# Optimization experiments

Hardware: AMD Instinct MI355X
Metric: run time of the kernel (lower is better)

Reference implementation:

```python
import jax, jax.numpy as jnp
import numpy as np

N_Q = 4
DEPTH = 6
DIM = 16  # 2**N_Q

# ---- fixed `design` dict (forward arg in the torch module; fixed here so the
# gate sequence is static, exercising every gate branch) ----
_K1 = ['x', 'y', 'z']
_K2 = ['H', 'Px', 'Py', 'Pz', 'CNot', 'CZ', 'Tof', 'CSwap']
DESIGN = {}
for _l in range(DEPTH):
    for _n in range(N_Q):
        DESIGN[str(_l) + str(_n) + '0'] = ((_l + _n) % 2 == 0)
        DESIGN[str(_l) + str(_n) + '1'] = _K1[(_l + _n) % 3]
        DESIGN[str(_l) + str(_n) + '2'] = _K2[(_l * N_Q + _n) % 8]

# ---- elementary gate matrices (numpy, build-time) ----
_H = np.array([[1, 1], [1, -1]], np.complex64) / np.sqrt(2.0)
_X = np.array([[0, 1], [1, 0]], np.complex64)
_Y = np.array([[0, -1j], [1j, 0]], np.complex64)
_Z = np.array([[1, 0], [0, -1]], np.complex64)
_CNOT = np.eye(4, dtype=np.complex64)[[0, 1, 3, 2]]
_CZ = np.diag(np.array([1, 1, 1, -1], np.complex64))
_TOF = np.eye(8, dtype=np.complex64)[[0, 1, 2, 3, 4, 5, 7, 6]]
_CSWAP = np.eye(8, dtype=np.complex64)[[0, 1, 2, 3, 4, 6, 5, 7]]


def _embed(gate, wires):
    # Embed a 2^k x 2^k gate acting on `wires` (wire 0 = most-significant bit,
    # PennyLane convention) into a full 16x16 unitary.
    k = len(wires)
    U = np.zeros((DIM, DIM), np.complex64)
    for i in range(DIM):
        bits = [(i >> (N_Q - 1 - q)) & 1 for q in range(N_Q)]
        sub_in = 0
        for w in wires:
            sub_in = (sub_in << 1) | bits[w]
        for sub_out in range(2 ** k):
            amp = gate[sub_out, sub_in]
            if amp != 0:
                ob = list(bits)
                for j, w in enumerate(wires):
                    ob[w] = (sub_out >> (k - 1 - j)) & 1
                o = 0
                for q in range(N_Q):
                    o = (o << 1) | ob[q]
                U[o, i] += amp
    return jnp.asarray(U)


# ---- static op list: ('fix', U16) | ('rot', kind, wire, angle_source) ----
_G1 = {'H': _H, 'Px': _X, 'Py': _Y, 'Pz': _Z}
OPS = [('fix', _embed(_H, [q])) for q in range(N_Q)]  # initial Hadamards
for _l in range(DEPTH):
    for _n in range(N_Q):
        if DESIGN[str(_l) + str(_n) + '0']:
            OPS.append(('rot', 'y', _n, ('x', _n)))  # RY(input feature)
        OPS.append(('rot', DESIGN[str(_l) + str(_n) + '1'], _n, ('w', _l, _n)))
        g = DESIGN[str(_l) + str(_n) + '2']
        if g in _G1:
            OPS.append(('fix', _embed(_G1[g], [_n])))
        elif g == 'CNot':
            OPS.append(('fix', _embed(_CNOT, [_n, (_n + 1) % N_Q])))
        elif g == 'CZ':
            OPS.append(('fix', _embed(_CZ, [_n, (_n + 1) % N_Q])))
        elif g == 'Tof':
            OPS.append(('fix', _embed(_TOF, [_n, (_n + 1) % N_Q, (_n + 2) % N_Q])))
        elif g == 'CSwap':
            OPS.append(('fix', _embed(_CSWAP, [_n, (_n + 1) % N_Q, (_n + 2) % N_Q])))


def _rot_mat(kind, th):
    # th: (B,) real angles -> (B,2,2) complex64 rotation matrices
    half = 0.5 * th
    c = jnp.cos(half).astype(jnp.complex64)
    s = jnp.sin(half).astype(jnp.complex64)
    if kind == 'x':
        m = [[c, (-1j) * s], [(-1j) * s, c]]
    elif kind == 'y':
        m = [[c, -s], [s, c]]
    else:  # 'z'
        e = jnp.exp((-1j) * half.astype(jnp.complex64))
        z = jnp.zeros_like(e)
        m = [[e, z], [z, jnp.conj(e)]]
    return jnp.stack([jnp.stack(m[0], -1), jnp.stack(m[1], -1)], -2)


def _apply_1q(state, M, q):
    # state: (B,16) complex, M: (B,2,2) complex, single-qubit gate on wire q
    B = state.shape[0]
    s = state.reshape(B, 2 ** q, 2, 2 ** (N_Q - 1 - q))
    s = jnp.einsum('bij,bajc->baic', M, s)
    return s.reshape(B, DIM)


def _run(state, x, w, adjoint):
    # adjoint: reversed gate order, negated rotation angles; all fixed gates
    # here (H, Paulis, CNOT, CZ, Toffoli, CSWAP) are Hermitian => self-adjoint.
    sign = -1.0 if adjoint else 1.0
    B = state.shape[0]
    for op in (reversed(OPS) if adjoint else OPS):
        if op[0] == 'fix':
            state = jnp.einsum('ij,bj->bi', op[1], state)
        else:
            _, kind, wire, src = op
            th = x[:, src[1]] if src[0] == 'x' else jnp.broadcast_to(w[src[1], src[2]], (B,))
            state = _apply_1q(state, _rot_mat(kind, sign * th), wire)
    return state


def _forward(x1, x2, q_params):
    w = q_params.reshape(DEPTH, N_Q)
    B = x1.shape[0]
    state = jnp.zeros((B, DIM), jnp.complex64).at[:, 0].set(1.0)
    state = _run(state, x1, w, False)   # quantum_net(x1, w)
    state = _run(state, x2, w, True)    # adjoint(quantum_net)(x2, w)
    a = state[:, 0]                     # probs[0] = |<0...0|psi>|^2
    return a.real ** 2 + a.imag ** 2


def setup_inputs():
    key = jax.random.key(0)
    k1, k2, k3 = jax.random.split(key, 3)
    B = 262144
    return {
        'x1': jax.random.normal(k1, (B, N_Q), jnp.float32),
        'x2': jax.random.normal(k2, (B, N_Q), jnp.float32),
        'q_params': jax.random.normal(k3, (DEPTH * N_Q,), jnp.float32),
    }


def reference(x1, x2, q_params):
    return _forward(x1, x2, q_params)
```

## Files before the change

### kernel.cpp

```cpp
#include <hip/hip_runtime.h>
#include <math.h>


#define DEVI static __device__ __forceinline__


template<int Q> DEVI void gH(float* vr, float* vi) {
  constexpr int m = 1 << (3 - Q);
  const float K = 0.70710678118654752440f;
#pragma unroll
  for (int i = 0; i < 16; ++i) if (!(i & m)) {
    const int j = i | m;
    float ar = vr[i], ai = vi[i], br = vr[j], bi = vi[j];
    vr[i] = (ar + br) * K; vi[i] = (ai + bi) * K;
    vr[j] = (ar - br) * K; vi[j] = (ai - bi) * K;
  }
}

template<int Q> DEVI void gX(float* vr, float* vi) {
  constexpr int m = 1 << (3 - Q);
#pragma unroll
  for (int i = 0; i < 16; ++i) if (!(i & m)) {
    const int j = i | m; float t;
    t = vr[i]; vr[i] = vr[j]; vr[j] = t;
    t = vi[i]; vi[i] = vi[j]; vi[j] = t;
  }
}

template<int Q> DEVI void gY(float* vr, float* vi) {
  constexpr int m = 1 << (3 - Q);
#pragma unroll
  for (int i = 0; i < 16; ++i) if (!(i & m)) {
    const int j = i | m;
    float ar = vr[i], ai = vi[i], br = vr[j], bi = vi[j];
    vr[i] = bi;  vi[i] = -br;
    vr[j] = -ai; vi[j] = ar;
  }
}

template<int Q> DEVI void gZ(float* vr, float* vi) {
  constexpr int m = 1 << (3 - Q);
#pragma unroll
  for (int i = 0; i < 16; ++i) if (i & m) { vr[i] = -vr[i]; vi[i] = -vi[i]; }
}

template<int Q> DEVI void gRY(float* vr, float* vi, float c, float s) {
  constexpr int m = 1 << (3 - Q);
#pragma unroll
  for (int i = 0; i < 16; ++i) if (!(i & m)) {
    const int j = i | m;
    float ar = vr[i], ai = vi[i], br = vr[j], bi = vi[j];
    vr[i] = c * ar - s * br; vi[i] = c * ai - s * bi;
    vr[j] = s * ar + c * br; vi[j] = s * ai + c * bi;
  }
}

template<int Q> DEVI void gRX(float* vr, float* vi, float c, float s) {
  constexpr int m = 1 << (3 - Q);
#pragma unroll
  for (int i = 0; i < 16; ++i) if (!(i & m)) {
    const int j = i | m;
    float ar = vr[i], ai = vi[i], br = vr[j], bi = vi[j];
    vr[i] = c * ar + s * bi; vi[i] = c * ai - s * br;
    vr[j] = c * br + s * ai; vi[j] = c * bi - s * ar;
  }
}

template<int Q> DEVI void gRZ(float* vr, float* vi, float c, float s) {
  constexpr int m = 1 << (3 - Q);
#pragma unroll
  for (int i = 0; i < 16; ++i) {
    float ar = vr[i], ai = vi[i];
    if (i & m) { vr[i] = c * ar - s * ai; vi[i] = c * ai + s * ar; }
    else       { vr[i] = c * ar + s * ai; vi[i] = c * ai - s * ar; }
  }
}

template<int C, int T> DEVI void gCNOT(float* vr, float* vi) {
  constexpr int mc = 1 << (3 - C), mt = 1 << (3 - T);
#pragma unroll
  for (int i = 0; i < 16; ++i) if ((i & mc) && !(i & mt)) {
    const int j = i | mt; float t;
    t = vr[i]; vr[i] = vr[j]; vr[j] = t;
    t = vi[i]; vi[i] = vi[j]; vi[j] = t;
  }
}

template<int A, int B2> DEVI void gCZ(float* vr, float* vi) {
  constexpr int ma = 1 << (3 - A), mb = 1 << (3 - B2);
#pragma unroll
  for (int i = 0; i < 16; ++i) if ((i & ma) && (i & mb)) { vr[i] = -vr[i]; vi[i] = -vi[i]; }
}

template<int C1, int C2, int T> DEVI void gTOF(float* vr, float* vi) {
  constexpr int m1 = 1 << (3 - C1), m2 = 1 << (3 - C2), mt = 1 << (3 - T);
#pragma unroll
  for (int i = 0; i < 16; ++i) if ((i & m1) && (i & m2) && !(i & mt)) {
    const int j = i | mt; float t;
    t = vr[i]; vr[i] = vr[j]; vr[j] = t;
    t = vi[i]; vi[i] = vi[j]; vi[j] = t;
  }
}

template<int C, int A, int B2> DEVI void gCSWAP(float* vr, float* vi) {
  constexpr int mc = 1 << (3 - C), ma = 1 << (3 - A), mb = 1 << (3 - B2);
#pragma unroll
  for (int i = 0; i < 16; ++i) if ((i & mc) && (i & ma) && !(i & mb)) {
    const int j = (i ^ ma) | mb; float t;
    t = vr[i]; vr[i] = vr[j]; vr[j] = t;
    t = vi[i]; vi[i] = vi[j]; vi[j] = t;
  }
}

__global__ void qprep(const float* __restrict__ q, float* __restrict__ wcs) {
  int k = threadIdx.x;
  if (k < 24) {
    float s, c;
    sincosf(0.5f * q[k], &s, &c);
    wcs[k] = c; wcs[24 + k] = s;
  }
}

template<bool WSPRE>
__global__ __launch_bounds__(256)
void qsim(const float* __restrict__ x1, const float* __restrict__ x2,
          const float* __restrict__ q, const float* __restrict__ wcs,
          float* __restrict__ out, int B)
{
  const int b = blockIdx.x * blockDim.x + threadIdx.x;
  if (b >= B) return;

  float cw[24], sw[24];
  if constexpr (WSPRE) {
#pragma unroll
    for (int k = 0; k < 24; ++k) { cw[k] = wcs[k]; sw[k] = wcs[24 + k]; }
  } else {
#pragma unroll
    for (int k = 0; k < 24; ++k) sincosf(0.5f * q[k], &sw[k], &cw[k]);
  }

  const float4 xa = reinterpret_cast<const float4*>(x1)[b];
  const float4 xb = reinterpret_cast<const float4*>(x2)[b];
  float ca[4], sa[4], cb[4], sb[4];
  sincosf(0.5f * xa.x, &sa[0], &ca[0]);
  sincosf(0.5f * xa.y, &sa[1], &ca[1]);
  sincosf(0.5f * xa.z, &sa[2], &ca[2]);
  sincosf(0.5f * xa.w, &sa[3], &ca[3]);
  sincosf(0.5f * xb.x, &sb[0], &cb[0]);
  sincosf(0.5f * xb.y, &sb[1], &cb[1]);
  sincosf(0.5f * xb.z, &sb[2], &cb[2]);
  sincosf(0.5f * xb.w, &sb[3], &cb[3]);

  float vr[16], vi[16];
#pragma unroll
  for (int i = 0; i < 16; ++i) { vr[i] = 0.f; vi[i] = 0.f; }
  vr[0] = 1.f;

  gH<0>(vr, vi); gH<1>(vr, vi); gH<2>(vr, vi); gH<3>(vr, vi);
  gRY<0>(vr, vi, ca[0], sa[0]); gRX<0>(vr, vi, cw[0],  sw[0]);  gH<0>(vr, vi);
  gRY<1>(vr, vi, cw[1], sw[1]); gX<1>(vr, vi);
  gRY<2>(vr, vi, ca[2], sa[2]); gRZ<2>(vr, vi, cw[2],  sw[2]);  gY<2>(vr, vi);
  gRX<3>(vr, vi, cw[3], sw[3]); gZ<3>(vr, vi);
  gRY<0>(vr, vi, cw[4], sw[4]); gCNOT<0,1>(vr, vi);
  gRY<1>(vr, vi, ca[1], sa[1]); gRZ<1>(vr, vi, cw[5],  sw[5]);  gCZ<1,2>(vr, vi);
  gRX<2>(vr, vi, cw[6], sw[6]); gTOF<2,3,0>(vr, vi);
  gRY<3>(vr, vi, ca[3], sa[3]); gRY<3>(vr, vi, cw[7],  sw[7]);  gCSWAP<3,0,1>(vr, vi);
  gRY<0>(vr, vi, ca[0], sa[0]); gRZ<0>(vr, vi, cw[8],  sw[8]);  gH<0>(vr, vi);
  gRX<1>(vr, vi, cw[9], sw[9]); gX<1>(vr, vi);
  gRY<2>(vr, vi, ca[2], sa[2]); gRY<2>(vr, vi, cw[10], sw[10]); gY<2>(vr, vi);
  gRZ<3>(vr, vi, cw[11], sw[11]); gZ<3>(vr, vi);
  gRX<0>(vr, vi, cw[12], sw[12]); gCNOT<0,1>(vr, vi);
  gRY<1>(vr, vi, ca[1], sa[1]); gRY<1>(vr, vi, cw[13], sw[13]); gCZ<1,2>(vr, vi);
  gRZ<2>(vr, vi, cw[14], sw[14]); gTOF<2,3,0>(vr, vi);
  gRY<3>(vr, vi, ca[3], sa[3]); gRX<3>(vr, vi, cw[15], sw[15]); gCSWAP<3,0,1>(vr, vi);
  gRY<0>(vr, vi, ca[0], sa[0]); gRY<0>(vr, vi, cw[16], sw[16]); gH<0>(vr, vi);
  gRZ<1>(vr, vi, cw[17], sw[17]); gX<1>(vr, vi);
  gRY<2>(vr, vi, ca[2], sa[2]); gRX<2>(vr, vi, cw[18], sw[18]); gY<2>(vr, vi);
  gRY<3>(vr, vi, cw[19], sw[19]); gZ<3>(vr, vi);
  gRZ<0>(vr, vi, cw[20], sw[20]); gCNOT<0,1>(vr, vi);
  gRY<1>(vr, vi, ca[1], sa[1]); gRX<1>(vr, vi, cw[21], sw[21]); gCZ<1,2>(vr, vi);
  gRY<2>(vr, vi, cw[22], sw[22]); gTOF<2,3,0>(vr, vi);
  gRY<3>(vr, vi, ca[3], sa[3]); gRZ<3>(vr, vi, cw[23], sw[23]); gCSWAP<3,0,1>(vr, vi);

  gCSWAP<3,0,1>(vr, vi); gRZ<3>(vr, vi, cw[23], -sw[23]); gRY<3>(vr, vi, cb[3], -sb[3]);
  gTOF<2,3,0>(vr, vi);   gRY<2>(vr, vi, cw[22], -sw[22]);
  gCZ<1,2>(vr, vi);      gRX<1>(vr, vi, cw[21], -sw[21]); gRY<1>(vr, vi, cb[1], -sb[1]);
  gCNOT<0,1>(vr, vi);    gRZ<0>(vr, vi, cw[20], -sw[20]);
  gZ<3>(vr, vi); gRY<3>(vr, vi, cw[19], -sw[19]);
  gY<2>(vr, vi); gRX<2>(vr, vi, cw[18], -sw[18]); gRY<2>(vr, vi, cb[2], -sb[2]);
  gX<1>(vr, vi); gRZ<1>(vr, vi, cw[17], -sw[17]);
  gH<0>(vr, vi); gRY<0>(vr, vi, cw[16], -sw[16]); gRY<0>(vr, vi, cb[0], -sb[0]);
  gCSWAP<3,0,1>(vr, vi); gRX<3>(vr, vi, cw[15], -sw[15]); gRY<3>(vr, vi, cb[3], -sb[3]);
  gTOF<2,3,0>(vr, vi);   gRZ<2>(vr, vi, cw[14], -sw[14]);
  gCZ<1,2>(vr, vi);      gRY<1>(vr, vi, cw[13], -sw[13]); gRY<1>(vr, vi, cb[1], -sb[1]);
  gCNOT<0,1>(vr, vi);    gRX<0>(vr, vi, cw[12], -sw[12]);
  gZ<3>(vr, vi); gRZ<3>(vr, vi, cw[11], -sw[11]);
  gY<2>(vr, vi); gRY<2>(vr, vi, cw[10], -sw[10]); gRY<2>(vr, vi, cb[2], -sb[2]);
  gX<1>(vr, vi); gRX<1>(vr, vi, cw[9],  -sw[9]);
  gH<0>(vr, vi); gRZ<0>(vr, vi, cw[8],  -sw[8]);  gRY<0>(vr, vi, cb[0], -sb[0]);
  gCSWAP<3,0,1>(vr, vi); gRY<3>(vr, vi, cw[7], -sw[7]); gRY<3>(vr, vi, cb[3], -sb[3]);
  gTOF<2,3,0>(vr, vi);   gRX<2>(vr, vi, cw[6], -sw[6]);
  gCZ<1,2>(vr, vi);      gRZ<1>(vr, vi, cw[5], -sw[5]); gRY<1>(vr, vi, cb[1], -sb[1]);
  gCNOT<0,1>(vr, vi);    gRY<0>(vr, vi, cw[4], -sw[4]);
  gZ<3>(vr, vi); gRX<3>(vr, vi, cw[3], -sw[3]);
  gY<2>(vr, vi); gRZ<2>(vr, vi, cw[2], -sw[2]); gRY<2>(vr, vi, cb[2], -sb[2]);
  gX<1>(vr, vi); gRY<1>(vr, vi, cw[1], -sw[1]);
  gH<0>(vr, vi); gRX<0>(vr, vi, cw[0], -sw[0]); gRY<0>(vr, vi, cb[0], -sb[0]);
  gH<3>(vr, vi); gH<2>(vr, vi); gH<1>(vr, vi); gH<0>(vr, vi);

  out[b] = vr[0] * vr[0] + vi[0] * vi[0];
}

extern "C" void kernel_launch(void* const* d_in, const int* in_sizes, int n_in,
                              void* d_out, int out_size, void* d_ws, size_t ws_size,
                              hipStream_t stream) {
  const float* x1 = (const float*)d_in[0];
  const float* x2 = (const float*)d_in[1];
  const float* q  = (const float*)d_in[2];
  float* out = (float*)d_out;
  const int B = in_sizes[0] / 4;
  const int block = 256;
  const int grid = (B + block - 1) / block;

  const bool use_ws = (d_ws != nullptr) && (ws_size >= 48 * sizeof(float));
  if (use_ws) {
    float* wcs = (float*)d_ws;
    qprep<<<1, 64, 0, stream>>>(q, wcs);
    qsim<true><<<grid, block, 0, stream>>>(x1, x2, q, wcs, out, B);
  } else {
    qsim<false><<<grid, block, 0, stream>>>(x1, x2, q, nullptr, out, B);
  }
}
```

Baseline: 93.81 us.

## Fuse weight sincos prep into main kernel, pack complex amplitudes, use fast sincos

```diff
diff --git a/kernel.cpp b/kernel.cpp
--- a/kernel.cpp
+++ b/kernel.cpp
@@ -4,211 +4,206 @@
 
 #define DEVI static __device__ __forceinline__
 
-
-template<int Q> DEVI void gH(float* vr, float* vi) {
+typedef float f2 __attribute__((ext_vector_type(2)));
+
+DEVI f2 nI(f2 a) { f2 r; r.x = a.y; r.y = -a.x; return r; }
+DEVI f2 pI(f2 a) { f2 r; r.x = -a.y; r.y = a.x; return r; }
+
+
+template<int Q> DEVI void gH(f2* v) {
   constexpr int m = 1 << (3 - Q);
   const float K = 0.70710678118654752440f;
 #pragma unroll
   for (int i = 0; i < 16; ++i) if (!(i & m)) {
     const int j = i | m;
-    float ar = vr[i], ai = vi[i], br = vr[j], bi = vi[j];
-    vr[i] = (ar + br) * K; vi[i] = (ai + bi) * K;
-    vr[j] = (ar - br) * K; vi[j] = (ai - bi) * K;
-  }
-}
-
-template<int Q> DEVI void gX(float* vr, float* vi) {
-  constexpr int m = 1 << (3 - Q);
-#pragma unroll
-  for (int i = 0; i < 16; ++i) if (!(i & m)) {
-    const int j = i | m; float t;
-    t = vr[i]; vr[i] = vr[j]; vr[j] = t;
-    t = vi[i]; vi[i] = vi[j]; vi[j] = t;
-  }
-}
-
-template<int Q> DEVI void gY(float* vr, float* vi) {
-  constexpr int m = 1 << (3 - Q);
-#pragma unroll
-  for (int i = 0; i < 16; ++i) if (!(i & m)) {
-    const int j = i | m;
-    float ar = vr[i], ai = vi[i], br = vr[j], bi = vi[j];
-    vr[i] = bi;  vi[i] = -br;
-    vr[j] = -ai; vi[j] = ar;
-  }
-}
-
-template<int Q> DEVI void gZ(float* vr, float* vi) {
-  constexpr int m = 1 << (3 - Q);
-#pragma unroll
-  for (int i = 0; i < 16; ++i) if (i & m) { vr[i] = -vr[i]; vi[i] = -vi[i]; }
-}
-
-template<int Q> DEVI void gRY(float* vr, float* vi, float c, float s) {
-  constexpr int m = 1 << (3 - Q);
-#pragma unroll
-  for (int i = 0; i < 16; ++i) if (!(i & m)) {
-    const int j = i | m;
-    float ar = vr[i], ai = vi[i], br = vr[j], bi = vi[j];
-    vr[i] = c * ar - s * br; vi[i] = c * ai - s * bi;
-    vr[j] = s * ar + c * br; vi[j] = s * ai + c * bi;
-  }
-}
-
-template<int Q> DEVI void gRX(float* vr, float* vi, float c, float s) {
-  constexpr int m = 1 << (3 - Q);
-#pragma unroll
-  for (int i = 0; i < 16; ++i) if (!(i & m)) {
-    const int j = i | m;
-    float ar = vr[i], ai = vi[i], br = vr[j], bi = vi[j];
-    vr[i] = c * ar + s * bi; vi[i] = c * ai - s * br;
-    vr[j] = c * br + s * ai; vi[j] = c * bi - s * ar;
-  }
-}
-
-template<int Q> DEVI void gRZ(float* vr, float* vi, float c, float s) {
+    f2 a = v[i], b = v[j];
+    v[i] = (a + b) * K;
+    v[j] = (a - b) * K;
+  }
+}
+
+template<int Q> DEVI void gX(f2* v) {
+  constexpr int m = 1 << (3 - Q);
+#pragma unroll
+  for (int i = 0; i < 16; ++i) if (!(i & m)) {
+    const int j = i | m;
+    f2 t = v[i]; v[i] = v[j]; v[j] = t;
+  }
+}
+
+template<int Q> DEVI void gY(f2* v) {
+  constexpr int m = 1 << (3 - Q);
+#pragma unroll
+  for (int i = 0; i < 16; ++i) if (!(i & m)) {
+    const int j = i | m;
+    f2 a = v[i], b = v[j];
+    v[i] = nI(b);
+    v[j] = pI(a);
+  }
+}
+
+template<int Q> DEVI void gZ(f2* v) {
+  constexpr int m = 1 << (3 - Q);
+#pragma unroll
+  for (int i = 0; i < 16; ++i) if (i & m) v[i] = -v[i];
+}
+
+template<int Q> DEVI void gRY(f2* v, float c, float s) {
+  constexpr int m = 1 << (3 - Q);
+#pragma unroll
+  for (int i = 0; i < 16; ++i) if (!(i & m)) {
+    const int j = i | m;
+    f2 a = v[i], b = v[j];
+    v[i] = a * c - b * s;
+    v[j] = a * s + b * c;
+  }
+}
+
+template<int Q> DEVI void gRX(f2* v, float c, float s) {
+  constexpr int m = 1 << (3 - Q);
+#pragma unroll
+  for (int i = 0; i < 16; ++i) if (!(i & m)) {
+    const int j = i | m;
+    f2 a = v[i], b = v[j];
+    v[i] = a * c + nI(b) * s;
+    v[j] = b * c + nI(a) * s;
+  }
+}
+
+template<int Q> DEVI void gRZ(f2* v, float c, float s) {
   constexpr int m = 1 << (3 - Q);
 #pragma unroll
   for (int i = 0; i < 16; ++i) {
-    float ar = vr[i], ai = vi[i];
-    if (i & m) { vr[i] = c * ar - s * ai; vi[i] = c * ai + s * ar; }
-    else       { vr[i] = c * ar + s * ai; vi[i] = c * ai - s * ar; }
-  }
-}
-
-template<int C, int T> DEVI void gCNOT(float* vr, float* vi) {
+    f2 a = v[i];
+    if (i & m) v[i] = a * c - nI(a) * s;
+    else       v[i] = a * c + nI(a) * s;
+  }
+}
+
+template<int C, int T> DEVI void gCNOT(f2* v) {
   constexpr int mc = 1 << (3 - C), mt = 1 << (3 - T);
 #pragma unroll
   for (int i = 0; i < 16; ++i) if ((i & mc) && !(i & mt)) {
-    const int j = i | mt; float t;
-    t = vr[i]; vr[i] = vr[j]; vr[j] = t;
-    t = vi[i]; vi[i] = vi[j]; vi[j] = t;
-  }
-}
-
-template<int A, int B2> DEVI void gCZ(float* vr, float* vi) {
+    const int j = i | mt;
+    f2 t = v[i]; v[i] = v[j]; v[j] = t;
+  }
+}
+
+template<int A, int B2> DEVI void gCZ(f2* v) {
   constexpr int ma = 1 << (3 - A), mb = 1 << (3 - B2);
 #pragma unroll
-  for (int i = 0; i < 16; ++i) if ((i & ma) && (i & mb)) { vr[i] = -vr[i]; vi[i] = -vi[i]; }
-}
-
-template<int C1, int C2, int T> DEVI void gTOF(float* vr, float* vi) {
+  for (int i = 0; i < 16; ++i) if ((i & ma) && (i & mb)) v[i] = -v[i];
+}
+
+template<int C1, int C2, int T> DEVI void gTOF(f2* v) {
   constexpr int m1 = 1 << (3 - C1), m2 = 1 << (3 - C2), mt = 1 << (3 - T);
 #pragma unroll
   for (int i = 0; i < 16; ++i) if ((i & m1) && (i & m2) && !(i & mt)) {
-    const int j = i | mt; float t;
-    t = vr[i]; vr[i] = vr[j]; vr[j] = t;
-    t = vi[i]; vi[i] = vi[j]; vi[j] = t;
-  }
-}
-
-template<int C, int A, int B2> DEVI void gCSWAP(float* vr, float* vi) {
+    const int j = i | mt;
+    f2 t = v[i]; v[i] = v[j]; v[j] = t;
+  }
+}
+
+template<int C, int A, int B2> DEVI void gCSWAP(f2* v) {
   constexpr int mc = 1 << (3 - C), ma = 1 << (3 - A), mb = 1 << (3 - B2);
 #pragma unroll
   for (int i = 0; i < 16; ++i) if ((i & mc) && (i & ma) && !(i & mb)) {
-    const int j = (i ^ ma) | mb; float t;
-    t = vr[i]; vr[i] = vr[j]; vr[j] = t;
-    t = vi[i]; vi[i] = vi[j]; vi[j] = t;
-  }
-}
-
-__global__ void qprep(const float* __restrict__ q, float* __restrict__ wcs) {
-  int k = threadIdx.x;
-  if (k < 24) {
-    float s, c;
-    sincosf(0.5f * q[k], &s, &c);
-    wcs[k] = c; wcs[24 + k] = s;
-  }
-}
-
-template<bool WSPRE>
+    const int j = (i ^ ma) | mb;
+    f2 t = v[i]; v[i] = v[j]; v[j] = t;
+  }
+}
+
+DEVI float rlane(float v, int l) {
+  return __int_as_float(__builtin_amdgcn_readlane(__float_as_int(v), l));
+}
+
 __global__ __launch_bounds__(256)
 void qsim(const float* __restrict__ x1, const float* __restrict__ x2,
-          const float* __restrict__ q, const float* __restrict__ wcs,
-          float* __restrict__ out, int B)
+          const float* __restrict__ q, float* __restrict__ out, int B)
 {
   const int b = blockIdx.x * blockDim.x + threadIdx.x;
   if (b >= B) return;
 
+  const int lane = threadIdx.x & 63;
+  float qv = 0.f;
+  if (lane < 24) qv = q[lane];
+  float mys, myc;
+  sincosf(0.5f * qv, &mys, &myc);
   float cw[24], sw[24];
-  if constexpr (WSPRE) {
-#pragma unroll
-    for (int k = 0; k < 24; ++k) { cw[k] = wcs[k]; sw[k] = wcs[24 + k]; }
-  } else {
-#pragma unroll
-    for (int k = 0; k < 24; ++k) sincosf(0.5f * q[k], &sw[k], &cw[k]);
-  }
+#pragma unroll
+  for (int k = 0; k < 24; ++k) { cw[k] = rlane(myc, k); sw[k] = rlane(mys, k); }
 
   const float4 xa = reinterpret_cast<const float4*>(x1)[b];
   const float4 xb = reinterpret_cast<const float4*>(x2)[b];
   float ca[4], sa[4], cb[4], sb[4];
-  sincosf(0.5f * xa.x, &sa[0], &ca[0]);
-  sincosf(0.5f * xa.y, &sa[1], &ca[1]);
-  sincosf(0.5f * xa.z, &sa[2], &ca[2]);
-  sincosf(0.5f * xa.w, &sa[3], &ca[3]);
-  sincosf(0.5f * xb.x, &sb[0], &cb[0]);
-  sincosf(0.5f * xb.y, &sb[1], &cb[1]);
-  sincosf(0.5f * xb.z, &sb[2], &cb[2]);
-  sincosf(0.5f * xb.w, &sb[3], &cb[3]);
-
-  float vr[16], vi[16];
-#pragma unroll
-  for (int i = 0; i < 16; ++i) { vr[i] = 0.f; vi[i] = 0.f; }
-  vr[0] = 1.f;
-
-  gH<0>(vr, vi); gH<1>(vr, vi); gH<2>(vr, vi); gH<3>(vr, vi);
-  gRY<0>(vr, vi, ca[0], sa[0]); gRX<0>(vr, vi, cw[0],  sw[0]);  gH<0>(vr, vi);
-  gRY<1>(vr, vi, cw[1], sw[1]); gX<1>(vr, vi);
-  gRY<2>(vr, vi, ca[2], sa[2]); gRZ<2>(vr, vi, cw[2],  sw[2]);  gY<2>(vr, vi);
-  gRX<3>(vr, vi, cw[3], sw[3]); gZ<3>(vr, vi);
-  gRY<0>(vr, vi, cw[4], sw[4]); gCNOT<0,1>(vr, vi);
-  gRY<1>(vr, vi, ca[1], sa[1]); gRZ<1>(vr, vi, cw[5],  sw[5]);  gCZ<1,2>(vr, vi);
-  gRX<2>(vr, vi, cw[6], sw[6]); gTOF<2,3,0>(vr, vi);
-  gRY<3>(vr, vi, ca[3], sa[3]); gRY<3>(vr, vi, cw[7],  sw[7]);  gCSWAP<3,0,1>(vr, vi);
-  gRY<0>(vr, vi, ca[0], sa[0]); gRZ<0>(vr, vi, cw[8],  sw[8]);  gH<0>(vr, vi);
-  gRX<1>(vr, vi, cw[9], sw[9]); gX<1>(vr, vi);
-  gRY<2>(vr, vi, ca[2], sa[2]); gRY<2>(vr, vi, cw[10], sw[10]); gY<2>(vr, vi);
-  gRZ<3>(vr, vi, cw[11], sw[11]); gZ<3>(vr, vi);
-  gRX<0>(vr, vi, cw[12], sw[12]); gCNOT<0,1>(vr, vi);
-  gRY<1>(vr, vi, ca[1], sa[1]); gRY<1>(vr, vi, cw[13], sw[13]); gCZ<1,2>(vr, vi);
-  gRZ<2>(vr, vi, cw[14], sw[14]); gTOF<2,3,0>(vr, vi);
-  gRY<3>(vr, vi, ca[3], sa[3]); gRX<3>(vr, vi, cw[15], sw[15]); gCSWAP<3,0,1>(vr, vi);
-  gRY<0>(vr, vi, ca[0], sa[0]); gRY<0>(vr, vi, cw[16], sw[16]); gH<0>(vr, vi);
-  gRZ<1>(vr, vi, cw[17], sw[17]); gX<1>(vr, vi);
-  gRY<2>(vr, vi, ca[2], sa[2]); gRX<2>(vr, vi, cw[18], sw[18]); gY<2>(vr, vi);
-  gRY<3>(vr, vi, cw[19], sw[19]); gZ<3>(vr, vi);
-  gRZ<0>(vr, vi, cw[20], sw[20]); gCNOT<0,1>(vr, vi);
-  gRY<1>(vr, vi, ca[1], sa[1]); gRX<1>(vr, vi, cw[21], sw[21]); gCZ<1,2>(vr, vi);
-  gRY<2>(vr, vi, cw[22], sw[22]); gTOF<2,3,0>(vr, vi);
-  gRY<3>(vr, vi, ca[3], sa[3]); gRZ<3>(vr, vi, cw[23], sw[23]); gCSWAP<3,0,1>(vr, vi);
-
-  gCSWAP<3,0,1>(vr, vi); gRZ<3>(vr, vi, cw[23], -sw[23]); gRY<3>(vr, vi, cb[3], -sb[3]);
-  gTOF<2,3,0>(vr, vi);   gRY<2>(vr, vi, cw[22], -sw[22]);
-  gCZ<1,2>(vr, vi);      gRX<1>(vr, vi, cw[21], -sw[21]); gRY<1>(vr, vi, cb[1], -sb[1]);
-  gCNOT<0,1>(vr, vi);    gRZ<0>(vr, vi, cw[20], -sw[20]);
-  gZ<3>(vr, vi); gRY<3>(vr, vi, cw[19], -sw[19]);
-  gY<2>(vr, vi); gRX<2>(vr, vi, cw[18], -sw[18]); gRY<2>(vr, vi, cb[2], -sb[2]);
-  gX<1>(vr, vi); gRZ<1>(vr, vi, cw[17], -sw[17]);
-  gH<0>(vr, vi); gRY<0>(vr, vi, cw[16], -sw[16]); gRY<0>(vr, vi, cb[0], -sb[0]);
-  gCSWAP<3,0,1>(vr, vi); gRX<3>(vr, vi, cw[15], -sw[15]); gRY<3>(vr, vi, cb[3], -sb[3]);
-  gTOF<2,3,0>(vr, vi);   gRZ<2>(vr, vi, cw[14], -sw[14]);
-  gCZ<1,2>(vr, vi);      gRY<1>(vr, vi, cw[13], -sw[13]); gRY<1>(vr, vi, cb[1], -sb[1]);
-  gCNOT<0,1>(vr, vi);    gRX<0>(vr, vi, cw[12], -sw[12]);
-  gZ<3>(vr, vi); gRZ<3>(vr, vi, cw[11], -sw[11]);
-  gY<2>(vr, vi); gRY<2>(vr, vi, cw[10], -sw[10]); gRY<2>(vr, vi, cb[2], -sb[2]);
-  gX<1>(vr, vi); gRX<1>(vr, vi, cw[9],  -sw[9]);
-  gH<0>(vr, vi); gRZ<0>(vr, vi, cw[8],  -sw[8]);  gRY<0>(vr, vi, cb[0], -sb[0]);
-  gCSWAP<3,0,1>(vr, vi); gRY<3>(vr, vi, cw[7], -sw[7]); gRY<3>(vr, vi, cb[3], -sb[3]);
-  gTOF<2,3,0>(vr, vi);   gRX<2>(vr, vi, cw[6], -sw[6]);
-  gCZ<1,2>(vr, vi);      gRZ<1>(vr, vi, cw[5], -sw[5]); gRY<1>(vr, vi, cb[1], -sb[1]);
-  gCNOT<0,1>(vr, vi);    gRY<0>(vr, vi, cw[4], -sw[4]);
-  gZ<3>(vr, vi); gRX<3>(vr, vi, cw[3], -sw[3]);
-  gY<2>(vr, vi); gRZ<2>(vr, vi, cw[2], -sw[2]); gRY<2>(vr, vi, cb[2], -sb[2]);
-  gX<1>(vr, vi); gRY<1>(vr, vi, cw[1], -sw[1]);
-  gH<0>(vr, vi); gRX<0>(vr, vi, cw[0], -sw[0]); gRY<0>(vr, vi, cb[0], -sb[0]);
-  gH<3>(vr, vi); gH<2>(vr, vi); gH<1>(vr, vi); gH<0>(vr, vi);
-
-  out[b] = vr[0] * vr[0] + vi[0] * vi[0];
+  __sincosf(0.5f * xa.x, &sa[0], &ca[0]);
+  __sincosf(0.5f * xa.y, &sa[1], &ca[1]);
+  __sincosf(0.5f * xa.z, &sa[2], &ca[2]);
+  __sincosf(0.5f * xa.w, &sa[3], &ca[3]);
+  __sincosf(0.5f * xb.x, &sb[0], &cb[0]);
+  __sincosf(0.5f * xb.y, &sb[1], &cb[1]);
+  __sincosf(0.5f * xb.z, &sb[2], &cb[2]);
+  __sincosf(0.5f * xb.w, &sb[3], &cb[3]);
+
+  f2 v[16];
+#pragma unroll
+  for (int i = 0; i < 16; ++i) { v[i].x = 0.f; v[i].y = 0.f; }
+  v[0].x = 1.f;
+
+  gH<0>(v); gH<1>(v); gH<2>(v); gH<3>(v);
+  gRY<0>(v, ca[0], sa[0]); gRX<0>(v, cw[0],  sw[0]);  gH<0>(v);
+  gRY<1>(v, cw[1], sw[1]); gX<1>(v);
+  gRY<2>(v, ca[2], sa[2]); gRZ<2>(v, cw[2],  sw[2]);  gY<2>(v);
+  gRX<3>(v, cw[3], sw[3]); gZ<3>(v);
+  gRY<0>(v, cw[4], sw[4]); gCNOT<0,1>(v);
+  gRY<1>(v, ca[1], sa[1]); gRZ<1>(v, cw[5],  sw[5]);  gCZ<1,2>(v);
+  gRX<2>(v, cw[6], sw[6]); gTOF<2,3,0>(v);
+  gRY<3>(v, ca[3], sa[3]); gRY<3>(v, cw[7],  sw[7]);  gCSWAP<3,0,1>(v);
+  gRY<0>(v, ca[0], sa[0]); gRZ<0>(v, cw[8],  sw[8]);  gH<0>(v);
+  gRX<1>(v, cw[9], sw[9]); gX<1>(v);
+  gRY<2>(v, ca[2], sa[2]); gRY<2>(v, cw[10], sw[10]); gY<2>(v);
+  gRZ<3>(v, cw[11], sw[11]); gZ<3>(v);
+  gRX<0>(v, cw[12], sw[12]); gCNOT<0,1>(v);
+  gRY<1>(v, ca[1], sa[1]); gRY<1>(v, cw[13], sw[13]); gCZ<1,2>(v);
+  gRZ<2>(v, cw[14], sw[14]); gTOF<2,3,0>(v);
+  gRY<3>(v, ca[3], sa[3]); gRX<3>(v, cw[15], sw[15]); gCSWAP<3,0,1>(v);
+  gRY<0>(v, ca[0], sa[0]); gRY<0>(v, cw[16], sw[16]); gH<0>(v);
+  gRZ<1>(v, cw[17], sw[17]); gX<1>(v);
+  gRY<2>(v, ca[2], sa[2]); gRX<2>(v, cw[18], sw[18]); gY<2>(v);
+  gRY<3>(v, cw[19], sw[19]); gZ<3>(v);
+  gRZ<0>(v, cw[20], sw[20]); gCNOT<0,1>(v);
+  gRY<1>(v, ca[1], sa[1]); gRX<1>(v, cw[21], sw[21]); gCZ<1,2>(v);
+  gRY<2>(v, cw[22], sw[22]); gTOF<2,3,0>(v);
+  gRY<3>(v, ca[3], sa[3]); gRZ<3>(v, cw[23], sw[23]); gCSWAP<3,0,1>(v);
+
+  gCSWAP<3,0,1>(v); gRZ<3>(v, cw[23], -sw[23]); gRY<3>(v, cb[3], -sb[3]);
+  gTOF<2,3,0>(v);   gRY<2>(v, cw[22], -sw[22]);
+  gCZ<1,2>(v);      gRX<1>(v, cw[21], -sw[21]); gRY<1>(v, cb[1], -sb[1]);
+  gCNOT<0,1>(v);    gRZ<0>(v, cw[20], -sw[20]);
+  gZ<3>(v); gRY<3>(v, cw[19], -sw[19]);
+  gY<2>(v); gRX<2>(v, cw[18], -sw[18]); gRY<2>(v, cb[2], -sb[2]);
+  gX<1>(v); gRZ<1>(v, cw[17], -sw[17]);
+  gH<0>(v); gRY<0>(v, cw[16], -sw[16]); gRY<0>(v, cb[0], -sb[0]);
+  gCSWAP<3,0,1>(v); gRX<3>(v, cw[15], -sw[15]); gRY<3>(v, cb[3], -sb[3]);
+  gTOF<2,3,0>(v);   gRZ<2>(v, cw[14], -sw[14]);
+  gCZ<1,2>(v);      gRY<1>(v, cw[13], -sw[13]); gRY<1>(v, cb[1], -sb[1]);
+  gCNOT<0,1>(v);    gRX<0>(v, cw[12], -sw[12]);
+  gZ<3>(v); gRZ<3>(v, cw[11], -sw[11]);
+  gY<2>(v); gRY<2>(v, cw[10], -sw[10]); gRY<2>(v, cb[2], -sb[2]);
+  gX<1>(v); gRX<1>(v, cw[9],  -sw[9]);
+  gH<0>(v); gRZ<0>(v, cw[8],  -sw[8]);  gRY<0>(v, cb[0], -sb[0]);
+  gCSWAP<3,0,1>(v); gRY<3>(v, cw[7], -sw[7]); gRY<3>(v, cb[3], -sb[3]);
+  gTOF<2,3,0>(v);   gRX<2>(v, cw[6], -sw[6]);
+  gCZ<1,2>(v);      gRZ<1>(v, cw[5], -sw[5]); gRY<1>(v, cb[1], -sb[1]);
+  gCNOT<0,1>(v);    gRY<0>(v, cw[4], -sw[4]);
+  gZ<3>(v); gRX<3>(v, cw[3], -sw[3]);
+  gY<2>(v); gRZ<2>(v, cw[2], -sw[2]); gRY<2>(v, cb[2], -sb[2]);
+  gX<1>(v); gRY<1>(v, cw[1], -sw[1]);
+  gH<0>(v); gRX<0>(v, cw[0], -sw[0]); gRY<0>(v, cb[0], -sb[0]);
+  gH<3>(v); gH<2>(v); gH<1>(v); gH<0>(v);
+
+  f2 a0 = v[0];
+  out[b] = a0.x * a0.x + a0.y * a0.y;
 }
 
 extern "C" void kernel_launch(void* const* d_in, const int* in_sizes, int n_in,
@@ -221,13 +216,5 @@
   const int B = in_sizes[0] / 4;
   const int block = 256;
   const int grid = (B + block - 1) / block;
-
-  const bool use_ws = (d_ws != nullptr) && (ws_size >= 48 * sizeof(float));
-  if (use_ws) {
-    float* wcs = (float*)d_ws;
-    qprep<<<1, 64, 0, stream>>>(q, wcs);
-    qsim<true><<<grid, block, 0, stream>>>(x1, x2, q, wcs, out, B);
-  } else {
-    qsim<false><<<grid, block, 0, stream>>>(x1, x2, q, nullptr, out, B);
-  }
-}
+  qsim<<<grid, block, 0, stream>>>(x1, x2, q, out, B);
+}
```

Measured after the change: 85.15 us. -9.2%, faster.
